# Kernel tuning notes

Hardware: AMD Instinct MI355X
Metric: run time of the kernel (lower is better)

The kernel has to match this reference:

```python
import jax, jax.numpy as jnp
import numpy as np

PAD, EOS, SOS = 0, 1, 2
V, E, H, B, T = 32000, 256, 512, 32, 64


def setup_inputs() -> dict:
    key = jax.random.key(0)
    ks = jax.random.split(key, 8)
    s_e = 1.0 / np.sqrt(H)
    emb = jax.random.normal(ks[0], (V, E), dtype=jnp.float32)
    emb = emb.at[PAD].set(0.0)  # padding_idx=PAD
    return {
        "hidden": jax.random.normal(ks[1], (1, B, H), dtype=jnp.float32),
        "emb": emb,
        "W_ih": jax.random.uniform(ks[2], (3 * H, E), minval=-s_e, maxval=s_e, dtype=jnp.float32),
        "W_hh": jax.random.uniform(ks[3], (3 * H, H), minval=-s_e, maxval=s_e, dtype=jnp.float32),
        "b_ih": jax.random.uniform(ks[4], (3 * H,), minval=-s_e, maxval=s_e, dtype=jnp.float32),
        "b_hh": jax.random.uniform(ks[5], (3 * H,), minval=-s_e, maxval=s_e, dtype=jnp.float32),
        "W_proj": jax.random.uniform(ks[6], (V, H), minval=-s_e, maxval=s_e, dtype=jnp.float32),
        "b_proj": jax.random.uniform(ks[7], (V,), minval=-s_e, maxval=s_e, dtype=jnp.float32),
        "max_len": T,
    }


def reference(hidden, emb, W_ih, W_hh, b_ih, b_hh, W_proj, b_proj, max_len):
    # Batched greedy GRU decode, equivalent to Decodeur.generate:
    # per-step: embed -> GRU cell -> linear proj -> argmax, feed back token.
    h0 = hidden[0]                                  # [B, H]
    nb = h0.shape[0]
    y0 = jnp.full((nb,), SOS, dtype=jnp.int32)
    done0 = jnp.zeros((nb,), dtype=bool)

    def step(carry, _):
        h, y, done = carry
        x = emb[y]                                  # [B, E]
        gx = x @ W_ih.T + b_ih                      # [B, 3H]
        gh = h @ W_hh.T + b_hh                      # [B, 3H]
        gxr, gxz, gxn = jnp.split(gx, 3, axis=-1)
        ghr, ghz, ghn = jnp.split(gh, 3, axis=-1)
        r = jax.nn.sigmoid(gxr + ghr)
        z = jax.nn.sigmoid(gxz + ghz)
        n = jnp.tanh(gxn + r * ghn)
        h_new = (1.0 - z) * n + z * h               # [B, H]
        logits = h_new @ W_proj.T + b_proj          # [B, V]
        y_new = jnp.argmax(logits, axis=-1).astype(jnp.int32)
        tok = jnp.where(done, EOS, y_new)           # pad with EOS once finished
        done_new = done | (y_new == EOS)
        return (h_new, tok, done_new), tok

    _, toks = jax.lax.scan(step, (h0, y0, done0), None, length=max_len)
    return toks                                     # [T, B] int32, EOS-padded
```

## Files before the change

### kernel.cpp

```cpp
#include <hip/hip_runtime.h>
#include <math.h>

#define EOS_TOK 1
#define SOS_TOK 2
#define Bn 32
#define Hn 512
#define En 256
#define Vn 32000
#define G3H 1536
#define NBLK 256
#define NTHR 1024
#define VPB 125
#define GPB 6
#define CE 0.0085f
#define LCAP 2048

typedef unsigned long long ull;
typedef unsigned int uint;
typedef __attribute__((ext_vector_type(8))) __bf16 bf16x8;
typedef __attribute__((ext_vector_type(4))) float f32x4;

union U4B { uint4 u; bf16x8 b; };
__device__ __forceinline__ bf16x8 u2b(uint4 u) { U4B x; x.u = u; return x.b; }

#define WBF_OFF 0ull
#define WN_OFF  32768000ull
#define GH_OFF  32896000ull
#define ES_OFF  33092608ull
#define LBS_OFF 33096704ull
#define DN_OFF  33100800ull
#define H_OFF   33101056ull

struct WS {
    unsigned short* wbf; float* wn; float* gh; ull* es; ull* lbs; int* done; float* h;
};
__device__ __forceinline__ WS get_ws(void* p) {
    WS w;
    w.wbf = (unsigned short*)((char*)p + WBF_OFF);
    w.wn  = (float*)((char*)p + WN_OFF);
    w.gh  = (float*)((char*)p + GH_OFF);
    w.es  = (ull*)((char*)p + ES_OFF);
    w.lbs = (ull*)((char*)p + LBS_OFF);
    w.done= (int*)((char*)p + DN_OFF);
    w.h   = (float*)((char*)p + H_OFF);
    return w;
}

template <typename T>
__device__ __forceinline__ T ldA(const T* p) {
    return __hip_atomic_load(p, __ATOMIC_RELAXED, __HIP_MEMORY_SCOPE_AGENT);
}
template <typename T>
__device__ __forceinline__ void stA(T* p, T v) {
    __hip_atomic_store(p, v, __ATOMIC_RELAXED, __HIP_MEMORY_SCOPE_AGENT);
}

struct PadCnt { ull v; ull pad[7]; };
__device__ PadCnt g_leaf[32];
__device__ ull    g_release;

__device__ __forceinline__ void grid_barrier(int bid) {
    __syncthreads();
    if (threadIdx.x == 0) {
        __builtin_amdgcn_s_waitcnt(0);
        ull my = __hip_atomic_fetch_add(&g_leaf[bid >> 3].v, 1ull,
                                        __ATOMIC_RELAXED, __HIP_MEMORY_SCOPE_AGENT) + 1;
        ull k = (my + 7) >> 3;
        if (bid == 0) {
            ull need = k << 3;
            for (;;) {
                bool again = false;
                #pragma unroll
                for (int i = 0; i < 32; ++i) again |= (ldA(&g_leaf[i].v) < need);
                if (!again) break;
                __builtin_amdgcn_s_sleep(1);
            }
            stA(&g_release, k);
        } else {
            while (ldA(&g_release) < k) __builtin_amdgcn_s_sleep(2);
        }
        __asm__ __volatile__("" ::: "memory");
    }
    __syncthreads();
}

__device__ __forceinline__ uint fkey(float f) {
    uint b = __float_as_uint(f);
    return (b & 0x80000000u) ? ~b : (b | 0x80000000u);
}
__device__ __forceinline__ float ifkey(uint k) {
    uint b = (k & 0x80000000u) ? (k ^ 0x80000000u) : ~k;
    return __uint_as_float(b);
}
__device__ __forceinline__ uint f2bf(float f) {
    uint u = __float_as_uint(f);
    return (u + 0x7FFFu + ((u >> 16) & 1u)) >> 16;
}
__device__ __forceinline__ float bflo(uint u) { return __uint_as_float(u << 16); }
__device__ __forceinline__ float bfhi(uint u) { return __uint_as_float(u & 0xFFFF0000u); }
__device__ __forceinline__ float ulo(ull u) { return __uint_as_float((uint)u); }
__device__ __forceinline__ float uhi(ull u) { return __uint_as_float((uint)(u >> 32)); }

struct SM {
    ull   hf[32 * 257];
    uint4 h4[2048];
    uint  lbk[32];
    float hn[32];
    float lbv2[32];
    float ghsc[GPB * 32 * 6];
    int   cnt; int pad0[3];
    unsigned short sidx[LCAP];
    float sU[LCAP];
    int   tok[32];
    float gx[192];
    float bpc[VPB + 3];
    float wnc[VPB + 3];
};

__device__ void prologue(int tid, int bid, const float* __restrict__ hidden,
                         const float* __restrict__ W_proj, WS w)
{
    for (int i = bid * NTHR + tid; i < Bn * Hn / 2; i += NBLK * NTHR)
        stA((ull*)w.h + i, ((const ull*)hidden)[i]);
    for (int i = bid * NTHR + tid; i < Vn * Hn / 4; i += NBLK * NTHR) {
        float4 v = ((const float4*)W_proj)[i];
        ull o = (ull)(f2bf(v.x) | (f2bf(v.y) << 16))
              | ((ull)(f2bf(v.z) | (f2bf(v.w) << 16)) << 32);
        stA((ull*)w.wbf + i, o);
    }
    for (int r = bid * NTHR + tid; r < Vn; r += NBLK * NTHR) {
        const float4* wr = (const float4*)(W_proj + (size_t)r * Hn);
        float s0 = 0.f, s1 = 0.f;
        for (int e = 0; e < 128; e += 2) {
            float4 a = wr[e], b4 = wr[e + 1];
            s0 += a.x * a.x + a.z * a.z + b4.x * b4.x + b4.z * b4.z;
            s1 += a.y * a.y + a.w * a.w + b4.y * b4.y + b4.w * b4.w;
        }
        stA(&w.wn[r], sqrtf(s0 + s1) * 1.0005f);
    }
}

__device__ __forceinline__ void stage_h(int tid, WS w, SM* sm) {
    for (int i = tid; i < 2048; i += NTHR) {
        int bb = i >> 6, e8 = i & 63;
        const ull* hs = (const ull*)w.h + bb * 256 + e8 * 4;
        ull a = ldA(hs), b2 = ldA(hs + 1), c = ldA(hs + 2), d = ldA(hs + 3);
        ull* hd = sm->hf + bb * 257 + e8 * 4;
        hd[0] = a; hd[1] = b2; hd[2] = c; hd[3] = d;
        uint4 P;
        P.x = f2bf(ulo(a))  | (f2bf(uhi(a))  << 16);
        P.y = f2bf(ulo(b2)) | (f2bf(uhi(b2)) << 16);
        P.z = f2bf(ulo(c))  | (f2bf(uhi(c))  << 16);
        P.w = f2bf(ulo(d))  | (f2bf(uhi(d))  << 16);
        sm->h4[(bb << 6) + (e8 ^ bb)] = P;
    }
}

__device__ void do_gh(int tid, int bid, const float* __restrict__ W_hh, SM* sm)
{
    if (tid < 832) return;
    int idx = tid - 832;
    int b = idx & 31, ks = idx >> 5;
    int f40 = ks * 21 + (ks < 2 ? ks : 2);
    int nf4 = 21 + (ks < 2 ? 1 : 0);
    const ull* hp = sm->hf + b * 257 + f40 * 2;
    const float4* wr[GPB];
    #pragma unroll
    for (int r6 = 0; r6 < GPB; ++r6)
        wr[r6] = (const float4*)(W_hh + (size_t)(bid * GPB + r6) * Hn) + f40;
    float p[GPB];
    #pragma unroll
    for (int r6 = 0; r6 < GPB; ++r6) p[r6] = 0.f;
    for (int e = 0; e < nf4; ++e) {
        ull u0 = hp[2 * e], u1 = hp[2 * e + 1];
        float h0 = ulo(u0), h1 = uhi(u0), h2 = ulo(u1), h3 = uhi(u1);
        #pragma unroll
        for (int r6 = 0; r6 < GPB; ++r6) {
            float4 wv4 = wr[r6][e];
            p[r6] += wv4.x * h0 + wv4.y * h1 + wv4.z * h2 + wv4.w * h3;
        }
    }
    #pragma unroll
    for (int r6 = 0; r6 < GPB; ++r6)
        sm->ghsc[(r6 * 32 + b) * 6 + ks] = p[r6];
}
__device__ void fin_gh(int tid, int base, int bid, const float* __restrict__ b_hh,
                       float* __restrict__ gh, SM* sm)
{
    if (tid >= base && tid < base + 192) {
        int idx = tid - base;
        int r6 = idx >> 5, b = idx & 31;
        float s = 0.f;
        #pragma unroll
        for (int j = 0; j < 6; ++j) s += sm->ghsc[(r6 * 32 + b) * 6 + j];
        int r = bid * GPB + r6;
        stA(&gh[(size_t)b * G3H + r], s + b_hh[r]);
    }
}

__device__ __forceinline__ void phase_bc(int tid, int bid, int t, WS w,
                         const float* __restrict__ W_hh, const float* __restrict__ b_hh,
                         const float* __restrict__ W_proj, const float* __restrict__ b_proj,
                         SM* sm)
{
    const int lane = tid & 63, wv = tid >> 6;

    stage_h(tid, w, sm);
    __syncthreads();

    do_gh(tid, bid, W_hh, sm);

    if (tid >= 800 && tid < 832) {
        int b = tid & 31;
        float s = 0.f;
        for (int e8 = 0; e8 < 64; ++e8) {
            uint4 H = sm->h4[(b << 6) + (e8 ^ b)];
            float f0=bflo(H.x),f1=bfhi(H.x),f2=bflo(H.y),f3=bfhi(H.y);
            float f4=bflo(H.z),f5=bfhi(H.z),f6=bflo(H.w),f7=bfhi(H.w);
            s += f0*f0+f1*f1+f2*f2+f3*f3+f4*f4+f5*f5+f6*f6+f7*f7;
        }
        sm->hn[b] = CE * sqrtf(s);
    }
    if (tid >= 512 && tid < 544) sm->lbk[tid - 512] = 0u;
    if (tid >= 544 && tid < 544 + VPB) {
        int rl = tid - 544;
        sm->bpc[rl] = b_proj[bid * VPB + rl];
        sm->wnc[rl] = w.wn[bid * VPB + rl];
    }
    if (tid == 672) sm->cnt = 0;

    f32x4 c0 = (f32x4){0.f,0.f,0.f,0.f}, c1 = (f32x4){0.f,0.f,0.f,0.f};
    if (wv < 8) {
        int arow = bid * VPB + wv * 16 + (lane & 15);
        if (arow > Vn - 1) arow = Vn - 1;
        const uint4* wp = (const uint4*)w.wbf + (size_t)arow * 64 + (lane >> 4);
        const int bb0 = lane & 15, bb1 = bb0 + 16;
        const int i0 = bb0 << 6, i1 = bb1 << 6;
        const int eb = lane >> 4;
        #pragma unroll
        for (int ks = 0; ks < 16; ++ks) {
            uint4 av = wp[ks * 4];
            int e8 = ks * 4 + eb;
            uint4 b0 = sm->h4[i0 + (e8 ^ bb0)];
            uint4 b1 = sm->h4[i1 + (e8 ^ bb1)];
            c0 = __builtin_amdgcn_mfma_f32_16x16x32_bf16(u2b(av), u2b(b0), c0, 0, 0, 0);
            c1 = __builtin_amdgcn_mfma_f32_16x16x32_bf16(u2b(av), u2b(b1), c1, 0, 0, 0);
        }
    }
    __syncthreads();

    const int rl0 = wv * 16 + ((lane >> 4) << 2);
    if (wv < 8) {
        ull k0 = 0ull, k1 = 0ull;
        const float hn0 = sm->hn[lane & 15], hn1 = sm->hn[(lane & 15) + 16];
        #pragma unroll
        for (int j = 0; j < 4; ++j) {
            int rl = rl0 + j;
            if (rl < VPB) {
                float bp = sm->bpc[rl], wn = sm->wnc[rl];
                ull q0 = ((ull)fkey(c0[j] + bp - hn0 * wn)) << 32;
                ull q1 = ((ull)fkey(c1[j] + bp - hn1 * wn)) << 32;
                if (q0 > k0) k0 = q0;
                if (q1 > k1) k1 = q1;
            }
        }
        ull o;
        o = __shfl_xor(k0, 16); if (o > k0) k0 = o;
        o = __shfl_xor(k0, 32); if (o > k0) k0 = o;
        o = __shfl_xor(k1, 16); if (o > k1) k1 = o;
        o = __shfl_xor(k1, 32); if (o > k1) k1 = o;
        if (lane < 16) atomicMax(&sm->lbk[lane], (uint)(k0 >> 32));
        else if (lane < 32) atomicMax(&sm->lbk[16 + (lane & 15)], (uint)(k1 >> 32));
    }
    __syncthreads();

    if (tid < Bn) {
        uint k = sm->lbk[tid];
        if (k) atomicMax(&w.lbs[((size_t)(t & 1) * 8 + (bid & 7)) * Bn + tid],
                         ((ull)k) << 32);
    }
    if (wv < 8) {
        #pragma unroll
        for (int tile = 0; tile < 2; ++tile) {
            const int b = (lane & 15) + (tile << 4);
            const float hnb = sm->hn[b], lb = ifkey(sm->lbk[b]);
            #pragma unroll
            for (int j = 0; j < 4; ++j) {
                int rl = rl0 + j;
                if (rl < VPB) {
                    float L = (tile ? c1[j] : c0[j]) + sm->bpc[rl];
                    float U = L + hnb * sm->wnc[rl];
                    if (U >= lb) {
                        int ix = atomicAdd(&sm->cnt, 1);
                        if (ix < LCAP) {
                            sm->sidx[ix] = (unsigned short)((rl << 5) | b);
                            sm->sU[ix] = U;
                        }
                    }
                }
            }
        }
    }
    fin_gh(tid, 512, bid, b_hh, w.gh, sm);
    __builtin_amdgcn_sched_barrier(0);
    if (tid < Bn) {
        const ull* sl = w.lbs + (size_t)(t & 1) * (8 * Bn);
        ull m = ldA(&sl[tid]);
        #pragma unroll
        for (int s = 1; s < 8; ++s) {
            ull v = ldA(&sl[s * Bn + tid]);
            if (v > m) m = v;
        }
        sm->lbv2[tid] = (m != 0ull) ? ifkey((uint)(m >> 32)) : -INFINITY;
    }
    __syncthreads();

    int nc = sm->cnt;
    if (nc <= LCAP) {
        for (int wi = wv; wi < nc; wi += 16) {
            uint e = sm->sidx[wi];
            int bb = (int)(e & 31);
            if (sm->sU[wi] < sm->lbv2[bb]) continue;
            int rl = (int)(e >> 5);
            int r = bid * VPB + rl;
            const float4* wr = (const float4*)(W_proj + (size_t)r * Hn) + lane * 2;
            float4 wA = wr[0], wB = wr[1];
            const ull* hp = sm->hf + bb * 257 + lane * 4;
            ull u0 = hp[0], u1 = hp[1], u2 = hp[2], u3 = hp[3];
            float s = wA.x*ulo(u0) + wA.y*uhi(u0) + wA.z*ulo(u1) + wA.w*uhi(u1)
                    + wB.x*ulo(u2) + wB.y*uhi(u2) + wB.z*ulo(u3) + wB.w*uhi(u3);
            #pragma unroll
            for (int d = 1; d < 64; d <<= 1) s += __shfl_xor(s, d);
            if (lane == 0) {
                s += sm->bpc[rl];
                ull q = ((ull)fkey(s) << 32) | (uint)(~(uint)r);
                atomicMax(&w.es[((size_t)(t & 1) * 8 + (bid & 7)) * Bn + bb], q);
            }
        }
    } else {
        for (int wi = wv; wi < VPB * Bn; wi += 16) {
            int rl = wi >> 5, bb = wi & 31;
            int r = bid * VPB + rl;
            const float4* wr = (const float4*)(W_proj + (size_t)r * Hn) + lane * 2;
            float4 wA = wr[0], wB = wr[1];
            const ull* hp = sm->hf + bb * 257 + lane * 4;
            ull u0 = hp[0], u1 = hp[1], u2 = hp[2], u3 = hp[3];
            float s = wA.x*ulo(u0) + wA.y*uhi(u0) + wA.z*ulo(u1) + wA.w*uhi(u1)
                    + wB.x*ulo(u2) + wB.y*uhi(u2) + wB.z*ulo(u3) + wB.w*uhi(u3);
            #pragma unroll
            for (int d = 1; d < 64; d <<= 1) s += __shfl_xor(s, d);
            if (lane == 0) {
                s += sm->bpc[rl];
                ull q = ((ull)fkey(s) << 32) | (uint)(~(uint)r);
                atomicMax(&w.es[((size_t)(t & 1) * 8 + (bid & 7)) * Bn + bb], q);
            }
        }
    }
}

__device__ __forceinline__ void phase_a(int tid, int bid, int t, int T,
                        const float* __restrict__ emb, const float* __restrict__ W_ih,
                        const float* __restrict__ b_ih, WS w, int* __restrict__ out, SM* sm)
{
    float ghr = 0.f, ghz = 0.f, ghn = 0.f;
    const int col_a = bid + ((tid >> 5) << 8);
    if (tid < 64 && t < T) {
        int b = tid & 31;
        const float* ghrow = w.gh + (size_t)b * G3H;
        ghr = ldA(&ghrow[col_a]);
        ghz = ldA(&ghrow[Hn + col_a]);
        ghn = ldA(&ghrow[2 * Hn + col_a]);
    }
    if (tid < Bn) {
        int b = tid, tok, dnew;
        if (t == 0) { tok = SOS_TOK; dnew = 0; }
        else {
            const ull* sl = w.es + (size_t)((t - 1) & 1) * (8 * Bn);
            ull m = ldA(&sl[b]);
            #pragma unroll
            for (int s = 1; s < 8; ++s) {
                ull v = ldA(&sl[s * Bn + b]);
                if (v > m) m = v;
            }
            int idx = (int)(~(uint)m);
            int dold = ldA(&w.done[((t - 1) & 1) * Bn + b]);
            tok = dold ? EOS_TOK : idx;
            dnew = dold | (idx == EOS_TOK);
        }
        sm->tok[b] = tok;
        if (bid == 0) {
            stA(&w.done[(t & 1) * Bn + b], dnew);
            if (t > 0) out[(size_t)(t - 1) * Bn + b] = tok;
            ull* s1 = w.es  + (size_t)(t & 1) * (8 * Bn);
            ull* s2 = w.lbs + (size_t)(t & 1) * (8 * Bn);
            #pragma unroll
            for (int s = 0; s < 8; ++s) { stA(&s1[s * Bn + b], 0ull); stA(&s2[s * Bn + b], 0ull); }
        }
    }
    __syncthreads();
    if (t >= T) return;

    if (tid < 768) {
        int d = tid >> 2, q = tid & 3;
        int b = d & 31, rem = d >> 5, gate = rem >> 1, ci = rem & 1;
        int col = bid + (ci << 8);
        const float* wrow = W_ih + (size_t)(gate * Hn + col) * En + q * (En / 4);
        const float* xrow = emb + (size_t)sm->tok[b] * En + q * (En / 4);
        float ax = 0.f, ay = 0.f;
        #pragma unroll
        for (int e4 = 0; e4 < En / 16; ++e4) {
            float4 w4 = *(const float4*)(wrow + 4 * e4);
            float4 x4 = *(const float4*)(xrow + 4 * e4);
            ax = fmaf(x4.x, w4.x, ax); ay = fmaf(x4.y, w4.y, ay);
            ax = fmaf(x4.z, w4.z, ax); ay = fmaf(x4.w, w4.w, ay);
        }
        float a = ax + ay;
        a += __shfl_xor(a, 1);
        a += __shfl_xor(a, 2);
        if (q == 0) sm->gx[(ci * 3 + gate) * 32 + b] = a;
    }
    __syncthreads();

    if (tid < 64) {
        int b = tid & 31, ci = tid >> 5;
        int col = col_a;
        float gxr = sm->gx[(ci * 3 + 0) * 32 + b] + b_ih[col];
        float gxz = sm->gx[(ci * 3 + 1) * 32 + b] + b_ih[Hn + col];
        float gxn = sm->gx[(ci * 3 + 2) * 32 + b] + b_ih[2 * Hn + col];
        float r = 1.0f / (1.0f + expf(-(gxr + ghr)));
        float z = 1.0f / (1.0f + expf(-(gxz + ghz)));
        float n = tanhf(gxn + r * ghn);
        float* hp = w.h + (size_t)b * Hn + col;
        float hold = ldA(hp);
        stA(hp, (1.0f - z) * n + z * hold);
    }
}

__global__ void __launch_bounds__(NTHR, 4)
decode_coop(const float* __restrict__ hidden, const float* __restrict__ emb,
            const float* __restrict__ W_ih, const float* __restrict__ W_hh,
            const float* __restrict__ b_ih, const float* __restrict__ b_hh,
            const float* __restrict__ W_proj, const float* __restrict__ b_proj,
            const int* __restrict__ max_len_p, int* __restrict__ out, void* ws_raw)
{
    const int tid = threadIdx.x, bid = blockIdx.x;
    __shared__ SM sm;
    WS w = get_ws(ws_raw);
    const int T = max_len_p[0];

    prologue(tid, bid, hidden, W_proj, w);
    grid_barrier(bid);
    stage_h(tid, w, &sm);
    __syncthreads();
    do_gh(tid, bid, W_hh, &sm);
    __syncthreads();
    fin_gh(tid, 0, bid, b_hh, w.gh, &sm);
    grid_barrier(bid);

    for (int t = 0; t < T; ++t) {
        phase_a(tid, bid, t, T, emb, W_ih, b_ih, w, out, &sm);
        grid_barrier(bid);
        phase_bc(tid, bid, t, w, W_hh, b_hh, W_proj, b_proj, &sm);
        grid_barrier(bid);
    }
    phase_a(tid, bid, T, T, emb, W_ih, b_ih, w, out, &sm);
}

__global__ void __launch_bounds__(NTHR, 4)
k_pro(const float* __restrict__ hidden, const float* __restrict__ W_proj, void* ws_raw) {
    WS w = get_ws(ws_raw);
    prologue(threadIdx.x, blockIdx.x, hidden, W_proj, w);
}
__global__ void __launch_bounds__(NTHR, 4)
k_pre(const float* __restrict__ W_hh, const float* __restrict__ b_hh, void* ws_raw) {
    __shared__ SM sm;
    WS w = get_ws(ws_raw);
    stage_h(threadIdx.x, w, &sm);
    __syncthreads();
    do_gh(threadIdx.x, blockIdx.x, W_hh, &sm);
    __syncthreads();
    fin_gh(threadIdx.x, 0, blockIdx.x, b_hh, w.gh, &sm);
}
__global__ void __launch_bounds__(NTHR, 4)
k_a(int t, const int* __restrict__ max_len_p,
    const float* __restrict__ emb, const float* __restrict__ W_ih,
    const float* __restrict__ b_ih, int* __restrict__ out, void* ws_raw)
{
    int T = max_len_p[0];
    if (t > T) return;
    __shared__ SM sm;
    WS w = get_ws(ws_raw);
    phase_a(threadIdx.x, blockIdx.x, t, T, emb, W_ih, b_ih, w, out, &sm);
}
__global__ void __launch_bounds__(NTHR, 4)
k_bc(int t, const int* __restrict__ max_len_p,
     const float* __restrict__ W_hh, const float* __restrict__ b_hh,
     const float* __restrict__ W_proj, const float* __restrict__ b_proj, void* ws_raw)
{
    if (t >= max_len_p[0]) return;
    __shared__ SM sm;
    WS w = get_ws(ws_raw);
    phase_bc(threadIdx.x, blockIdx.x, t, w, W_hh, b_hh, W_proj, b_proj, &sm);
}

extern "C" void kernel_launch(void* const* d_in, const int* in_sizes, int n_in,
                              void* d_out, int out_size, void* d_ws, size_t ws_size,
                              hipStream_t stream) {
    const float* hidden = (const float*)d_in[0];
    const float* emb    = (const float*)d_in[1];
    const float* W_ih   = (const float*)d_in[2];
    const float* W_hh   = (const float*)d_in[3];
    const float* b_ih   = (const float*)d_in[4];
    const float* b_hh   = (const float*)d_in[5];
    const float* W_proj = (const float*)d_in[6];
    const float* b_proj = (const float*)d_in[7];
    const int* max_len  = (const int*)d_in[8];
    int* out = (int*)d_out;
    void* ws = d_ws;

    void* args[] = {&hidden, &emb, &W_ih, &W_hh, &b_ih, &b_hh,
                    &W_proj, &b_proj, &max_len, &out, &ws};
    hipError_t err = hipLaunchCooperativeKernel((const void*)decode_coop,
                                                dim3(NBLK), dim3(NTHR), args, 0, stream);
    if (err != hipSuccess) {
        (void)hipGetLastError();
        hipLaunchKernelGGL(k_pro, dim3(NBLK), dim3(NTHR), 0, stream, hidden, W_proj, ws);
        hipLaunchKernelGGL(k_pre, dim3(NBLK), dim3(NTHR), 0, stream, W_hh, b_hh, ws);
        for (int t = 0; t <= 64; ++t) {
            hipLaunchKernelGGL(k_a, dim3(NBLK), dim3(NTHR), 0, stream,
                               t, max_len, emb, W_ih, b_ih, out, ws);
            if (t < 64) {
                hipLaunchKernelGGL(k_bc, dim3(NBLK), dim3(NTHR), 0, stream,
                                   t, max_len, W_hh, b_hh, W_proj, b_proj, ws);
            }
        }
    }
}
```

Measured before the change: 3.945 ms.

## Distribute barrier release flags and compact exact-rescore candidates before two-per-wave processing

The grid barrier's single release word becomes 32 padded per-group release flags, so each group of eight blocks polls its own cache line instead of all blocks contending on one address. The exact fp32 rescoring pass first filters candidates against the lower bound into a compacted list in shared memory. Each wave then handles two surviving candidates per iteration, interleaving their loads and shuffle reductions. The cost is an extra block-wide sync plus shared-memory atomics for compaction, and block 0 now issues 32 stores on each release.

```diff
diff --git a/kernel.cpp b/kernel.cpp
--- a/kernel.cpp
+++ b/kernel.cpp
@@ -57,7 +57,7 @@
 
 struct PadCnt { ull v; ull pad[7]; };
 __device__ PadCnt g_leaf[32];
-__device__ ull    g_release;
+__device__ PadCnt g_rel[32];
 
 __device__ __forceinline__ void grid_barrier(int bid) {
     __syncthreads();
@@ -75,9 +75,11 @@
                 if (!again) break;
                 __builtin_amdgcn_s_sleep(1);
             }
-            stA(&g_release, k);
+            #pragma unroll
+            for (int i = 0; i < 32; ++i) stA(&g_rel[i].v, k);
         } else {
-            while (ldA(&g_release) < k) __builtin_amdgcn_s_sleep(2);
+            const ull* myrel = &g_rel[bid >> 3].v;
+            while (ldA(myrel) < k) __builtin_amdgcn_s_sleep(2);
         }
         __asm__ __volatile__("" ::: "memory");
     }
@@ -108,9 +110,10 @@
     float hn[32];
     float lbv2[32];
     float ghsc[GPB * 32 * 6];
-    int   cnt; int pad0[3];
+    int   cnt; int cnt2; int pad0[2];
     unsigned short sidx[LCAP];
     float sU[LCAP];
+    unsigned short sidx2[LCAP];
     int   tok[32];
     float gx[192];
     float bpc[VPB + 3];
@@ -228,6 +231,7 @@
         sm->wnc[rl] = w.wn[bid * VPB + rl];
     }
     if (tid == 672) sm->cnt = 0;
+    if (tid == 673) sm->cnt2 = 0;
 
     f32x4 c0 = (f32x4){0.f,0.f,0.f,0.f}, c1 = (f32x4){0.f,0.f,0.f,0.f};
     if (wv < 8) {
@@ -317,24 +321,48 @@
 
     int nc = sm->cnt;
     if (nc <= LCAP) {
-        for (int wi = wv; wi < nc; wi += 16) {
-            uint e = sm->sidx[wi];
-            int bb = (int)(e & 31);
-            if (sm->sU[wi] < sm->lbv2[bb]) continue;
-            int rl = (int)(e >> 5);
-            int r = bid * VPB + rl;
-            const float4* wr = (const float4*)(W_proj + (size_t)r * Hn) + lane * 2;
-            float4 wA = wr[0], wB = wr[1];
-            const ull* hp = sm->hf + bb * 257 + lane * 4;
-            ull u0 = hp[0], u1 = hp[1], u2 = hp[2], u3 = hp[3];
-            float s = wA.x*ulo(u0) + wA.y*uhi(u0) + wA.z*ulo(u1) + wA.w*uhi(u1)
-                    + wB.x*ulo(u2) + wB.y*uhi(u2) + wB.z*ulo(u3) + wB.w*uhi(u3);
+        for (int i = tid; i < nc; i += NTHR) {
+            uint e = sm->sidx[i];
+            if (sm->sU[i] >= sm->lbv2[e & 31]) {
+                int j = atomicAdd(&sm->cnt2, 1);
+                sm->sidx2[j] = (unsigned short)e;
+            }
+        }
+        __syncthreads();
+        int nc2 = sm->cnt2;
+        for (int wi = wv; wi < nc2; wi += 32) {
+            uint eA = sm->sidx2[wi];
+            int wiB = wi + 16;
+            bool hasB = wiB < nc2;
+            uint eB = hasB ? sm->sidx2[wiB] : eA;
+            int rlA = (int)(eA >> 5), bbA = (int)(eA & 31);
+            int rlB = (int)(eB >> 5), bbB = (int)(eB & 31);
+            const float4* wrA = (const float4*)(W_proj + (size_t)(bid * VPB + rlA) * Hn) + lane * 2;
+            const float4* wrB = (const float4*)(W_proj + (size_t)(bid * VPB + rlB) * Hn) + lane * 2;
+            float4 a0 = wrA[0], a1 = wrA[1];
+            float4 b0 = wrB[0], b1 = wrB[1];
+            const ull* hpA = sm->hf + bbA * 257 + lane * 4;
+            const ull* hpB = sm->hf + bbB * 257 + lane * 4;
+            ull ua0 = hpA[0], ua1 = hpA[1], ua2 = hpA[2], ua3 = hpA[3];
+            ull ub0 = hpB[0], ub1 = hpB[1], ub2 = hpB[2], ub3 = hpB[3];
+            float sA = a0.x*ulo(ua0) + a0.y*uhi(ua0) + a0.z*ulo(ua1) + a0.w*uhi(ua1)
+                     + a1.x*ulo(ua2) + a1.y*uhi(ua2) + a1.z*ulo(ua3) + a1.w*uhi(ua3);
+            float sB = b0.x*ulo(ub0) + b0.y*uhi(ub0) + b0.z*ulo(ub1) + b0.w*uhi(ub1)
+                     + b1.x*ulo(ub2) + b1.y*uhi(ub2) + b1.z*ulo(ub3) + b1.w*uhi(ub3);
             #pragma unroll
-            for (int d = 1; d < 64; d <<= 1) s += __shfl_xor(s, d);
+            for (int d = 1; d < 64; d <<= 1) {
+                sA += __shfl_xor(sA, d);
+                sB += __shfl_xor(sB, d);
+            }
             if (lane == 0) {
-                s += sm->bpc[rl];
-                ull q = ((ull)fkey(s) << 32) | (uint)(~(uint)r);
-                atomicMax(&w.es[((size_t)(t & 1) * 8 + (bid & 7)) * Bn + bb], q);
+                int rA = bid * VPB + rlA;
+                ull qA = ((ull)fkey(sA + sm->bpc[rlA]) << 32) | (uint)(~(uint)rA);
+                atomicMax(&w.es[((size_t)(t & 1) * 8 + (bid & 7)) * Bn + bbA], qA);
+                if (hasB) {
+                    int rB = bid * VPB + rlB;
+                    ull qB = ((ull)fkey(sB + sm->bpc[rlB]) << 32) | (uint)(~(uint)rB);
+                    atomicMax(&w.es[((size_t)(t & 1) * 8 + (bid & 7)) * Bn + bbB], qB);
+                }
             }
         }
     } else {
```

After: 4.086 ms. +3.6%, slower.
